# Optimization experiments

Measured on AMD Instinct MI355X. Metric: run time of the kernel, lower is better.

## Reference

```python
import jax, jax.numpy as jnp
import numpy as np

B, H, N, D = 2, 8, 2048, 64


def setup_inputs() -> dict:
    key = jax.random.key(0)
    kq, kk, kv = jax.random.split(key, 3)
    q = jax.random.normal(kq, (B, H, N, D), dtype=jnp.float32)
    k = jax.random.normal(kk, (B, H, N, D), dtype=jnp.float32)
    v = jax.random.normal(kv, (B, H, N, D), dtype=jnp.float32)
    return {"q": q, "k": k, "v": v}


def _selective_attn(sim):
    # sim: (b, h, i, j). Gate computed from first head, relu'd, SOS unmasked,
    # diagonal zeroed, shifted down one row, cumsum over query rows, subtracted.
    b, h, i, j = sim.shape
    gate = jax.nn.relu(sim[:, 0])                       # (b, i, j)
    gate = gate.at[:, :, j - i].set(0.0)                # no_mask_sos: column -i
    eye = jnp.eye(i, dtype=sim.dtype)
    if j > i:
        eye = jnp.pad(eye, ((0, 0), (j - i, 0)), constant_values=1.0)
    gate = (1.0 - eye) * gate
    # F.pad(gate, (0,0,1,-1)): shift rows down by one, drop last row
    gate = jnp.pad(gate, ((0, 0), (1, 0), (0, 0)))[:, :i, :]
    gate = jnp.cumsum(gate, axis=-2)
    return sim - gate[:, None]                          # broadcast over heads


def reference(q, k, v):
    scale = q.shape[-1] ** -0.5
    i, j = q.shape[-2], k.shape[-2]

    # squared L2 distance scores: ||q||^2 + ||k||^2 - 2 q.k  (== cdist(q,k)**2)
    q_sq = jnp.sum(q * q, axis=-1)                      # (b, h, i)
    k_sq = jnp.sum(k * k, axis=-1)                      # (b, h, j)
    qk = jnp.einsum('bhid,bhjd->bhij', q, k)            # (b, h, i, j)
    d2 = jnp.maximum(q_sq[..., :, None] + k_sq[..., None, :] - 2.0 * qk, 0.0)
    sim = -d2 * scale

    # causal mask (triu with offset j - i + 1)
    mask_value = -jnp.finfo(sim.dtype).max
    causal = jnp.triu(jnp.ones((i, j), dtype=bool), j - i + 1)
    sim = jnp.where(causal, mask_value, sim)

    # selective attention gating
    sim = _selective_attn(sim)

    # one-hot straight-through attention
    idx = jnp.argmax(sim, axis=-1)                      # (b, h, i)
    hard = jax.nn.one_hot(idx, j, dtype=sim.dtype)      # (b, h, i, j)
    soft = jax.nn.softmax(sim, axis=-1)
    attn = hard + soft - jax.lax.stop_gradient(soft)

    return jnp.einsum('bhij,bhjd->bhid', attn, v)
```

## Files before the change

### kernel.cpp

```cpp
#include <hip/hip_runtime.h>
#include <stdint.h>

#define B_ 2
#define H_ 8
#define N_ 2048
#define D_ 64
#define BH_ (B_ * H_)
#define NROWS (BH_ * N_)
#define TPB_ 576
#define TASKS (TPB_ * BH_)
#define EPSF 8e-3f
#define INFF __int_as_float(0x7f800000)

using u64 = unsigned long long;
using u32 = unsigned int;
typedef __attribute__((ext_vector_type(8))) short short8;
typedef __attribute__((ext_vector_type(4))) float f32x4;

#define MFMA16(A, B, C) __builtin_amdgcn_mfma_f32_16x16x32_bf16((A), (B), (C), 0, 0, 0)

__global__ __launch_bounds__(256) void prep_k(
    const float* __restrict__ k, char* __restrict__ khi_g,
    char* __restrict__ klo_g, float* __restrict__ ksq_g,
    u32* __restrict__ count)
{
  if (blockIdx.x == 0 && threadIdx.x == 0) count[0] = 0;
  const int t = (int)blockIdx.x * 256 + threadIdx.x;
  const int r = t >> 3, kg = t & 7;
  const float* kp = k + (size_t)r * D_ + kg * 8;
  const float4 f0 = *(const float4*)kp;
  const float4 f1 = *(const float4*)(kp + 4);
  const float vv[8] = {f0.x, f0.y, f0.z, f0.w, f1.x, f1.y, f1.z, f1.w};
  u32 hw[4], lw[4];
  float ps = 0.f;
  #pragma unroll
  for (int e = 0; e < 4; ++e) {
    const float va = vv[2 * e], vb = vv[2 * e + 1];
    ps = fmaf(va, va, ps); ps = fmaf(vb, vb, ps);
    const u32 ha = __float_as_uint(va) & 0xFFFF0000u;
    const u32 hb = __float_as_uint(vb) & 0xFFFF0000u;
    hw[e] = (ha >> 16) | hb;
    const u32 la = __float_as_uint(va - __uint_as_float(ha));
    const u32 lb = __float_as_uint(vb - __uint_as_float(hb));
    lw[e] = (la >> 16) | (lb & 0xFFFF0000u);
  }
  const size_t off = ((size_t)(r >> 4) * 2 + (kg >> 2)) * 1024 +
                     (size_t)(((kg & 3) << 4) + (r & 15)) * 16;
  *(uint4*)(khi_g + off) = make_uint4(hw[0], hw[1], hw[2], hw[3]);
  *(uint4*)(klo_g + off) = make_uint4(lw[0], lw[1], lw[2], lw[3]);
  float ssum = ps;
  ssum += __shfl_xor(ssum, 1);
  ssum += __shfl_xor(ssum, 2);
  ssum += __shfl_xor(ssum, 4);
  if (kg == 0) ksq_g[r] = ssum;
}

__device__ __forceinline__ void cvt_hilo(const float* p, short8& hi, short8& lo) {
  const float4 f0 = *(const float4*)p;
  const float4 f1 = *(const float4*)(p + 4);
  const float vv[8] = {f0.x, f0.y, f0.z, f0.w, f1.x, f1.y, f1.z, f1.w};
  #pragma unroll
  for (int e = 0; e < 8; ++e) {
    const float v = vv[e];
    const u32 hb = __float_as_uint(v) & 0xFFFF0000u;
    hi[e] = (short)(hb >> 16);
    lo[e] = (short)(__float_as_uint(v - __uint_as_float(hb)) >> 16);
  }
}

__global__ __launch_bounds__(64, 6) void phase1(
    const float* __restrict__ q, const char* __restrict__ khi_g,
    const char* __restrict__ klo_g, const float* __restrict__ ksq_g,
    u64* __restrict__ bestc, u32* __restrict__ secc)
{
  const int b = (int)blockIdx.x;
  const int task = (b & 7) * (TASKS / 8) + (b >> 3);
  const int bh = task / TPB_;
  const int rem = task - bh * TPB_;
  int m = 0;
  while (8 * (m + 1) * (m + 2) <= rem) ++m;
  const int idx = rem - 8 * m * (m + 1);
  const int qn = idx / (m + 1);
  const int g1 = 16 * m + qn;
  const int c = idx - qn * (m + 1);
  const int jfirst = c * 16;
  const int jlast = min(jfirst + 15, g1);

  const int lane = threadIdx.x & 63;
  const int grp = lane >> 4, c0 = lane & 15;
  const int i0 = g1 * 16;

  short8 ah0, ah1, al0, al1;
  {
    const float* q0 = q + ((size_t)bh * N_ + i0 + c0) * D_ + grp * 8;
    cvt_hilo(q0, ah0, al0);
    cvt_hilo(q0 + 32, ah1, al1);
  }

  float bf[4], sf[4];
  u32 bj[4];
  #pragma unroll
  for (int r2 = 0; r2 < 4; ++r2) {
    bf[r2] = INFF; sf[r2] = INFF; bj[r2] = 0;
  }

  const size_t fb = (size_t)bh * 128 * 2048;
  const char* ph = khi_g + fb + (size_t)jfirst * 2048 + lane * 16;
  const char* pl = klo_g + fb + (size_t)jfirst * 2048 + lane * 16;
  const float* pk = ksq_g + (size_t)bh * N_ + jfirst * 16 + c0;

  for (int js = jfirst; js <= jlast; ++js) {
    const short8 ch0 = *(const short8*)(ph);
    const short8 ch1 = *(const short8*)(ph + 1024);
    const short8 cl0 = *(const short8*)(pl);
    const short8 cl1 = *(const short8*)(pl + 1024);
    const float cks = *pk;
    ph += 2048; pl += 2048; pk += 16;

    const int jcol = js * 16 + c0;
    const bool dsub = (js == g1);
    f32x4 aA = {0.f, 0.f, 0.f, 0.f}, aB = {0.f, 0.f, 0.f, 0.f};
    aA = MFMA16(ah0, ch0, aA);  aB = MFMA16(ah1, ch1, aB);
    aA = MFMA16(ah0, cl0, aA);  aB = MFMA16(ah1, cl1, aB);
    aA = MFMA16(al0, ch0, aA);  aB = MFMA16(al1, ch1, aB);
    #pragma unroll
    for (int reg = 0; reg < 4; ++reg) {
      float score = fmaf(-2.f, aA[reg] + aB[reg], cks);
      if (dsub && jcol > i0 + grp * 4 + reg) score = INFF;
      const float loser = fmaxf(bf[reg], score);
      sf[reg] = fminf(sf[reg], loser);
      if (score < bf[reg]) bj[reg] = (u32)jcol;
      bf[reg] = fminf(bf[reg], score);
    }
  }

  #pragma unroll
  for (int reg = 0; reg < 4; ++reg) {
    const u32 bbits = __float_as_uint(bf[reg]);
    const u32 key = bbits ^ (u32)(((int)bbits >> 31) | 0x80000000);
    u64 pkk = ((u64)key << 32) | bj[reg];
    float sv = sf[reg];
    #pragma unroll
    for (int mm = 1; mm < 16; mm <<= 1) {
      const u64 opk = (u64)__shfl_xor((long long)pkk, mm);
      const float osv = __shfl_xor(sv, mm);
      const u32 mk = (u32)(pkk >> 32), ok = (u32)(opk >> 32);
      const u32 lk = (opk < pkk) ? mk : ok;
      const u32 lb = (lk & 0x80000000u) ? (lk ^ 0x80000000u) : ~lk;
      sv = fminf(fminf(sv, osv), __uint_as_float(lb));
      if (opk < pkk) pkk = opk;
    }
    if (c0 == 0) {
      const size_t rr = (size_t)bh * N_ + i0 + grp * 4 + reg;
      bestc[(size_t)c * NROWS + rr] = pkk;
      secc[(size_t)c * NROWS + rr] = __float_as_uint(sv);
    }
  }
}

__global__ __launch_bounds__(256) void combine_gather(
    const u64* __restrict__ bestc, const u32* __restrict__ secc,
    const float* __restrict__ v, float* __restrict__ out,
    u32* __restrict__ flaglist, u32* __restrict__ count)
{
  __shared__ u64 pk_s[4][64];
  __shared__ float s1_s[4][64];
  __shared__ u32 idx_s[64];
  const int tid = threadIdx.x;
  const int r0 = (int)blockIdx.x * 64;
  const int p = tid >> 6, t6 = tid & 63;

  {
    const int r = r0 + t6;
    const int i = r & (N_ - 1);
    const int nch = ((i >> 4) + 16) >> 4;
    u64 b0 = ~0ull;
    float bcur = INFF, s1 = INFF;
    int cstar = -1;
    for (int c2 = p; c2 < nch; c2 += 4) {
      const u64 kk = bestc[(size_t)c2 * NROWS + r];
      const u32 key = (u32)(kk >> 32);
      const u32 bits = (key & 0x80000000u) ? (key ^ 0x80000000u) : ~key;
      const float f = __uint_as_float(bits);
      if (kk < b0) { s1 = fminf(s1, bcur); b0 = kk; bcur = f; cstar = c2; }
      else s1 = fminf(s1, f);
    }
    if (cstar >= 0)
      s1 = fminf(s1, __uint_as_float(secc[(size_t)cstar * NROWS + r]));
    pk_s[p][t6] = b0;
    s1_s[p][t6] = s1;
  }
  __syncthreads();

  if (tid < 64) {
    u64 b0 = ~0ull;
    float bcur = INFF, s1 = INFF;
    #pragma unroll
    for (int pp = 0; pp < 4; ++pp) {
      const u64 kk = pk_s[pp][tid];
      const u32 key = (u32)(kk >> 32);
      const u32 bits = (key & 0x80000000u) ? (key ^ 0x80000000u) : ~key;
      const float f = __uint_as_float(bits);
      if (kk < b0) { s1 = fminf(s1, bcur); b0 = kk; bcur = f; }
      else s1 = fminf(s1, f);
      s1 = fminf(s1, s1_s[pp][tid]);
    }
    idx_s[tid] = (u32)(b0 & 0xFFFFu);
    if ((s1 - bcur) < EPSF) {
      const u32 pos = atomicAdd(count, 1u);
      flaglist[pos] = (u32)(r0 + tid);
    }
  }
  __syncthreads();

  #pragma unroll
  for (int iter = 0; iter < 4; ++iter) {
    const int tk = tid + iter * 256;
    const int rl = tk >> 4, cc = tk & 15;
    const int r = r0 + rl;
    const u32 j = idx_s[rl];
    const int bh = r >> 11;
    const float4 val = ((const float4*)(v + ((size_t)bh * N_ + j) * D_))[cc];
    ((float4*)(out + (size_t)r * D_))[cc] = val;
  }
}

__global__ __launch_bounds__(64) void exact_partial(
    const float* __restrict__ q, const float* __restrict__ k,
    const u32* __restrict__ flaglist, const u32* __restrict__ count,
    double* __restrict__ pd, int* __restrict__ pj)
{
  const int lane = threadIdx.x & 63;
  const int cnt = (int)count[0];
  for (int t = blockIdx.x; (t >> 4) < cnt; t += (int)gridDim.x) {
    const int li = t >> 4, slice = t & 15;
    const int r = (int)flaglist[li];
    const int bh = r >> 11;
    const int i = r & (N_ - 1);
    const int jbase = slice * 128;

    double bbest = 1e300;
    int bjj = 0x7FFFFFFF;
    if (jbase <= i) {
      const float4* qr = (const float4*)(q + (size_t)r * D_);
      float4 qv[16];
      #pragma unroll
      for (int t2 = 0; t2 < 16; ++t2) qv[t2] = qr[t2];
      double s0 = 0, s1 = 0, s2 = 0, s3 = 0;
      #pragma unroll
      for (int t2 = 0; t2 < 16; ++t2) {
        s0 = fma((double)qv[t2].x, (double)qv[t2].x, s0);
        s1 = fma((double)qv[t2].y, (double)qv[t2].y, s1);
        s2 = fma((double)qv[t2].z, (double)qv[t2].z, s2);
        s3 = fma((double)qv[t2].w, (double)qv[t2].w, s3);
      }
      const double qsqd = (s0 + s1) + (s2 + s3);
      const float* kb = k + (size_t)bh * N_ * D_;

      #pragma unroll
      for (int u = 0; u < 2; ++u) {
        const int j = jbase + u * 64 + lane;
        if (j <= i) {
          const float4* kr = (const float4*)(kb + (size_t)j * D_);
          double a0 = 0, a1 = 0, a2 = 0, a3 = 0;
          double t0 = 0, t1 = 0, t2d = 0, t3 = 0;
          #pragma unroll
          for (int t2 = 0; t2 < 16; ++t2) {
            const float4 kv = kr[t2];
            const double k0 = kv.x, k1 = kv.y, k2 = kv.z, k3 = kv.w;
            a0 = fma((double)qv[t2].x, k0, a0);
            a1 = fma((double)qv[t2].y, k1, a1);
            a2 = fma((double)qv[t2].z, k2, a2);
            a3 = fma((double)qv[t2].w, k3, a3);
            t0 = fma(k0, k0, t0);
            t1 = fma(k1, k1, t1);
            t2d = fma(k2, k2, t2d);
            t3 = fma(k3, k3, t3);
          }
          const double raw = (qsqd + ((t0 + t1) + (t2d + t3))) -
                             2.0 * ((a0 + a1) + (a2 + a3));
          const double d2 = raw > 0.0 ? raw : 0.0;
          if (d2 < bbest) { bbest = d2; bjj = j; }
        }
      }
      #pragma unroll
      for (int mm = 1; mm < 64; mm <<= 1) {
        const double ob = __shfl_xor(bbest, mm);
        const int oj = __shfl_xor(bjj, mm);
        if (ob < bbest || (ob == bbest && oj < bjj)) { bbest = ob; bjj = oj; }
      }
    }
    if (lane == 0) {
      pd[(size_t)li * 16 + slice] = bbest;
      pj[(size_t)li * 16 + slice] = bjj;
    }
  }
}

__global__ __launch_bounds__(64) void exact_final(
    const double* __restrict__ pd, const int* __restrict__ pj,
    const u32* __restrict__ flaglist, const u32* __restrict__ count,
    const float* __restrict__ v, float* __restrict__ out)
{
  const int lane = threadIdx.x & 63;
  const int cnt = (int)count[0];
  for (int li = blockIdx.x; li < cnt; li += (int)gridDim.x) {
    const int r = (int)flaglist[li];
    const int bh = r >> 11;
    double d = (lane < 16) ? pd[(size_t)li * 16 + lane] : 1e300;
    int j = (lane < 16) ? pj[(size_t)li * 16 + lane] : 0x7FFFFFFF;
    #pragma unroll
    for (int mm = 1; mm < 16; mm <<= 1) {
      const double od = __shfl_xor(d, mm);
      const int oj = __shfl_xor(j, mm);
      if (od < d || (od == d && oj < j)) { d = od; j = oj; }
    }
    if (lane < 16) {
      const float4 val =
          ((const float4*)(v + ((size_t)bh * N_ + j) * D_))[lane];
      ((float4*)(out + (size_t)r * D_))[lane] = val;
    }
  }
}

extern "C" void kernel_launch(void* const* d_in, const int* in_sizes, int n_in,
                              void* d_out, int out_size, void* d_ws,
                              size_t ws_size, hipStream_t stream) {
  const float* q = (const float*)d_in[0];
  const float* k = (const float*)d_in[1];
  const float* v = (const float*)d_in[2];
  float* out = (float*)d_out;

  char* ws = (char*)d_ws;
  u32* count = (u32*)ws;
  u32* flaglist = (u32*)(ws + 4096);
  float* ksq_g = (float*)(ws + 256 * 1024);
  char* khi_g = ws + 1ull * 1024 * 1024;
  char* klo_g = ws + 8ull * 1024 * 1024;
  u64* bestc = (u64*)(ws + 16ull * 1024 * 1024);
  u32* secc = (u32*)(ws + 24ull * 1024 * 1024);
  double* pd = (double*)(ws + 32ull * 1024 * 1024);
  int* pj = (int*)(ws + 40ull * 1024 * 1024);

  prep_k<<<(NROWS * 8) / 256, 256, 0, stream>>>(k, khi_g, klo_g, ksq_g, count);
  phase1<<<TASKS, 64, 0, stream>>>(q, khi_g, klo_g, ksq_g, bestc, secc);
  combine_gather<<<NROWS / 64, 256, 0, stream>>>(bestc, secc, v, out,
                                                 flaglist, count);
  exact_partial<<<2048, 64, 0, stream>>>(q, k, flaglist, count, pd, pj);
  exact_final<<<256, 64, 0, stream>>>(pd, pj, flaglist, count, v, out);
}
```

Before: 54.12 us.

## Interleave K hi/lo bf16 tiles into one buffer and raise phase1 occupancy

The separate hi and lo bf16 split buffers for K are merged into one interleaved buffer, so each 16-row key tile's hi and lo halves sit together in one contiguous 4KB block. Phase1 then walks a single pointer with one stride, which should give more contiguous memory access and fewer address registers. The launch bound's minimum blocks per CU goes from 6 to 8, which may limit registers per thread and could cause spills.

```diff
diff --git a/kernel.cpp b/kernel.cpp
--- a/kernel.cpp
+++ b/kernel.cpp
@@ -20,9 +20,8 @@
 #define MFMA16(A, B, C) __builtin_amdgcn_mfma_f32_16x16x32_bf16((A), (B), (C), 0, 0, 0)
 
 __global__ __launch_bounds__(256) void prep_k(
-    const float* __restrict__ k, char* __restrict__ khi_g,
-    char* __restrict__ klo_g, float* __restrict__ ksq_g,
-    u32* __restrict__ count)
+    const float* __restrict__ k, char* __restrict__ kf_g,
+    float* __restrict__ ksq_g, u32* __restrict__ count)
 {
   if (blockIdx.x == 0 && threadIdx.x == 0) count[0] = 0;
   const int t = (int)blockIdx.x * 256 + threadIdx.x;
@@ -44,10 +43,10 @@
     const u32 lb = __float_as_uint(vb - __uint_as_float(hb));
     lw[e] = (la >> 16) | (lb & 0xFFFF0000u);
   }
-  const size_t off = ((size_t)(r >> 4) * 2 + (kg >> 2)) * 1024 +
-                     (size_t)(((kg & 3) << 4) + (r & 15)) * 16;
-  *(uint4*)(khi_g + off) = make_uint4(hw[0], hw[1], hw[2], hw[3]);
-  *(uint4*)(klo_g + off) = make_uint4(lw[0], lw[1], lw[2], lw[3]);
+  const size_t base = (size_t)(r >> 4) * 4096 + (size_t)(kg >> 2) * 1024 +
+                      (size_t)(((kg & 3) << 4) + (r & 15)) * 16;
+  *(uint4*)(kf_g + base) = make_uint4(hw[0], hw[1], hw[2], hw[3]);
+  *(uint4*)(kf_g + base + 2048) = make_uint4(lw[0], lw[1], lw[2], lw[3]);
   float ssum = ps;
   ssum += __shfl_xor(ssum, 1);
   ssum += __shfl_xor(ssum, 2);
@@ -68,9 +67,9 @@
   }
 }
 
-__global__ __launch_bounds__(64, 6) void phase1(
-    const float* __restrict__ q, const char* __restrict__ khi_g,
-    const char* __restrict__ klo_g, const float* __restrict__ ksq_g,
+__global__ __launch_bounds__(64, 8) void phase1(
+    const float* __restrict__ q, const char* __restrict__ kf_g,
+    const float* __restrict__ ksq_g,
     u64* __restrict__ bestc, u32* __restrict__ secc)
 {
   const int b = (int)blockIdx.x;
@@ -104,18 +103,17 @@
     bf[r2] = INFF; sf[r2] = INFF; bj[r2] = 0;
   }
 
-  const size_t fb = (size_t)bh * 128 * 2048;
-  const char* ph = khi_g + fb + (size_t)jfirst * 2048 + lane * 16;
-  const char* pl = klo_g + fb + (size_t)jfirst * 2048 + lane * 16;
+  const char* pf = kf_g + (size_t)bh * 128 * 4096 +
+                   (size_t)jfirst * 4096 + lane * 16;
   const float* pk = ksq_g + (size_t)bh * N_ + jfirst * 16 + c0;
 
   for (int js = jfirst; js <= jlast; ++js) {
-    const short8 ch0 = *(const short8*)(ph);
-    const short8 ch1 = *(const short8*)(ph + 1024);
-    const short8 cl0 = *(const short8*)(pl);
-    const short8 cl1 = *(const short8*)(pl + 1024);
+    const short8 ch0 = *(const short8*)(pf);
+    const short8 ch1 = *(const short8*)(pf + 1024);
+    const short8 cl0 = *(const short8*)(pf + 2048);
+    const short8 cl1 = *(const short8*)(pf + 3072);
     const float cks = *pk;
-    ph += 2048; pl += 2048; pk += 16;
+    pf += 4096; pk += 16;
 
     const int jcol = js * 16 + c0;
     const bool dsub = (js == g1);
@@ -335,15 +333,14 @@
   u32* count = (u32*)ws;
   u32* flaglist = (u32*)(ws + 4096);
   float* ksq_g = (float*)(ws + 256 * 1024);
-  char* khi_g = ws + 1ull * 1024 * 1024;
-  char* klo_g = ws + 8ull * 1024 * 1024;
+  char* kf_g = ws + 1ull * 1024 * 1024;
   u64* bestc = (u64*)(ws + 16ull * 1024 * 1024);
   u32* secc = (u32*)(ws + 24ull * 1024 * 1024);
   double* pd = (double*)(ws + 32ull * 1024 * 1024);
   int* pj = (int*)(ws + 40ull * 1024 * 1024);
 
-  prep_k<<<(NROWS * 8) / 256, 256, 0, stream>>>(k, khi_g, klo_g, ksq_g, count);
-  phase1<<<TASKS, 64, 0, stream>>>(q, khi_g, klo_g, ksq_g, bestc, secc);
+  prep_k<<<(NROWS * 8) / 256, 256, 0, stream>>>(k, kf_g, ksq_g, count);
+  phase1<<<TASKS, 64, 0, stream>>>(q, kf_g, ksq_g, bestc, secc);
   combine_gather<<<NROWS / 64, 256, 0, stream>>>(bestc, secc, v, out,
                                                  flaglist, count);
   exact_partial<<<2048, 64, 0, stream>>>(q, k, flaglist, count, pd, pj);
```

Measured after the change: 54.96 us. No clear change (+1.5%).
